# Optimization experiments

Hardware: AMD Instinct MI355X
Metric: run time of the kernel (lower is better)

Reference implementation:

```python
import jax, jax.numpy as jnp
import numpy as np

NUM_HEADS = 8
DIM_HEAD = 48
SCALE = DIM_HEAD ** -0.5


def setup_inputs() -> dict:
    key = jax.random.key(0)
    k1, k2, k3 = jax.random.split(key, 3)
    B, N, D = 4, 2048, 384
    inner = NUM_HEADS * DIM_HEAD  # 384
    x = jax.random.normal(k1, (B, N, D), dtype=jnp.float32)
    # store weights in [in, out] layout (equivalent to torch Linear W.T)
    Wqkv = jax.random.normal(k2, (D, 3 * inner), dtype=jnp.float32) * (D ** -0.5)
    Wproj = jax.random.normal(k3, (inner, D), dtype=jnp.float32) * (inner ** -0.5)
    bproj = jnp.zeros((D,), dtype=jnp.float32)
    return {"x": x, "Wqkv": Wqkv, "Wproj": Wproj, "bproj": bproj}


def reference(x, Wqkv, Wproj, bproj):
    B, N, D = x.shape
    h, dh = NUM_HEADS, DIM_HEAD
    C = h * dh
    # fused QKV projection (qkv_bias=False)
    qkv = (x @ Wqkv).reshape(B, N, 3, h, dh)
    q = qkv[:, :, 0].transpose(0, 2, 1, 3)  # [B, h, N, dh]
    k = qkv[:, :, 1].transpose(0, 2, 1, 3)
    v = qkv[:, :, 2].transpose(0, 2, 1, 3)
    # naive attention: materialize [B, h, N, N] scores
    sim = jnp.einsum("bhqd,bhkd->bhqk", q, k) * SCALE
    attn = jax.nn.softmax(sim, axis=-1)
    out = jnp.einsum("bhqk,bhkd->bhqd", attn, v)  # [B, h, N, dh]
    out = out.transpose(0, 2, 1, 3).reshape(B, N, C)
    return out @ Wproj + bproj
```

## Files before the change

### kernel.cpp

```cpp
#include <hip/hip_runtime.h>
#include <hip/hip_bf16.h>


typedef _Float16 f16x8 __attribute__((ext_vector_type(8)));
typedef _Float16 f16x4 __attribute__((ext_vector_type(4)));
typedef _Float16 f16x2 __attribute__((ext_vector_type(2)));
typedef float    f32x4 __attribute__((ext_vector_type(4)));
typedef float    f32x16 __attribute__((ext_vector_type(16)));

#define QSCL 0.20822035963448658f

static __device__ __forceinline__ f16x2 cvt_pk_f16(float a, float b) {
    return __builtin_bit_cast(f16x2, __builtin_amdgcn_cvt_pkrtz(a, b));
}

__global__ __launch_bounds__(256) void prep(const float4* __restrict__ x,
                                            const float* __restrict__ wq,
                                            const float* __restrict__ wp,
                                            f16x4* __restrict__ xh4,
                                            _Float16* __restrict__ wqt,
                                            _Float16* __restrict__ wpt)
{
    __shared__ _Float16 t[64][65];
    const int blk = blockIdx.x, tid = threadIdx.x;
    if (blk < 144) {
        const float* src; _Float16* dst; int Nn, k0, n0;
        if (blk < 108) {
            src = wq; dst = wqt; Nn = 1152;
            k0 = (blk % 6) * 64; n0 = (blk / 6) * 64;
        } else {
            const int b2 = blk - 108;
            src = wp; dst = wpt; Nn = 384;
            k0 = (b2 % 6) * 64; n0 = (b2 / 6) * 64;
        }
        #pragma unroll
        for (int i = 0; i < 16; i++) {
            const int id = tid + i * 256;
            const int k = id >> 6, n = id & 63;
            t[k][n] = (_Float16)src[(size_t)(k0 + k) * Nn + n0 + n];
        }
        __syncthreads();
        #pragma unroll
        for (int i = 0; i < 16; i++) {
            const int id = tid + i * 256;
            const int n = id >> 6, k = id & 63;
            dst[(size_t)(n0 + n) * 384 + k0 + k] = t[k][n];
        }
    } else {
        const int base = (blk - 144) * 3072;
        #pragma unroll
        for (int r = 0; r < 12; r++) {
            const int j = base + r * 256 + tid;
            const float4 tt = x[j];
            f16x4 hh;
            hh[0] = (_Float16)tt.x; hh[1] = (_Float16)tt.y;
            hh[2] = (_Float16)tt.z; hh[3] = (_Float16)tt.w;
            xh4[j] = hh;
        }
    }
}

union QkvSmem {
    struct { _Float16 As[128][40]; _Float16 Bs[128][40]; } g;
    _Float16 Ts[128][136];
    _Float16 Ts2[128][136];
};

__global__ __launch_bounds__(256) void qkv_f16(const _Float16* __restrict__ A,
                                               const _Float16* __restrict__ Bt,
                                               _Float16* __restrict__ qh,
                                               _Float16* __restrict__ kh,
                                               _Float16* __restrict__ vt)
{
    __shared__ QkvSmem sm;
    const int tid = threadIdx.x;
    const int w = tid >> 6, lane = tid & 63, cl = lane & 15, quad = lane >> 4;
    const int bm = blockIdx.x, bn = blockIdx.y;

    f32x4 acc[2][8];
    const f32x4 z4 = {0.f, 0.f, 0.f, 0.f};
    #pragma unroll
    for (int mi = 0; mi < 2; mi++)
        #pragma unroll
        for (int t = 0; t < 8; t++) acc[mi][t] = z4;

    const int ar = tid >> 2, ac = (tid & 3) * 8;
    const _Float16* Ag = A  + (size_t)(bm * 128 + ar) * 384 + ac;
    const _Float16* Bg = Bt + (size_t)(bn * 128 + ar) * 384 + ac;

    f16x8 pa[2], pb[2];
    #pragma unroll
    for (int j = 0; j < 2; j++) {
        pa[j] = *(const f16x8*)(Ag + (size_t)(64 * j) * 384);
        pb[j] = *(const f16x8*)(Bg + (size_t)(64 * j) * 384);
    }

    for (int k0 = 0; k0 < 384; k0 += 32) {
        __syncthreads();
        #pragma unroll
        for (int j = 0; j < 2; j++) {
            *(f16x8*)&sm.g.As[ar + 64 * j][ac] = pa[j];
            *(f16x8*)&sm.g.Bs[ar + 64 * j][ac] = pb[j];
        }
        __syncthreads();
        if (k0 + 32 < 384) {
            #pragma unroll
            for (int j = 0; j < 2; j++) {
                pa[j] = *(const f16x8*)(Ag + (size_t)(64 * j) * 384 + k0 + 32);
                pb[j] = *(const f16x8*)(Bg + (size_t)(64 * j) * 384 + k0 + 32);
            }
        }
        f16x8 bf[8];
        #pragma unroll
        for (int t = 0; t < 8; t++)
            bf[t] = *(const f16x8*)&sm.g.Bs[t * 16 + cl][quad * 8];
        #pragma unroll
        for (int mi = 0; mi < 2; mi++) {
            const f16x8 af = *(const f16x8*)&sm.g.As[w * 32 + mi * 16 + cl][quad * 8];
            #pragma unroll
            for (int t = 0; t < 8; t++)
                acc[mi][t] = __builtin_amdgcn_mfma_f32_16x16x32_f16(af, bf[t], acc[mi][t], 0, 0, 0);
        }
    }

    const int s = (bn * 128) / 384;
    const int b  = (bm * 128) >> 11;
    const int n0 = (bm * 128) & 2047;
    if (s == 2) {
        __syncthreads();
        const int qp = ((quad & 1) << 1) | (quad >> 1);
        #pragma unroll
        for (int t = 0; t < 8; t++)
            #pragma unroll
            for (int mi = 0; mi < 2; mi++)
                #pragma unroll
                for (int r = 0; r < 4; r++)
                    sm.Ts[t * 16 + cl][w * 32 + mi * 16 + qp * 4 + r] =
                        (_Float16)acc[mi][t][r];
        __syncthreads();
        const int colbase = bn * 128 - 768;
        #pragma unroll
        for (int i = 0; i < 8; i++) {
            const int c = i * 256 + tid;
            const int col = c >> 4, nc = c & 15;
            const int gcol = colbase + col;
            const int head = gcol / 48, d = gcol - head * 48;
            const int bh = b * 8 + head;
            *(f16x8*)&vt[(size_t)(bh * 48 + d) * 2048 + n0 + nc * 8] =
                *(const f16x8*)&sm.Ts[col][nc * 8];
        }
    } else {
        __syncthreads();
        const float scl = (s == 0) ? QSCL : 1.0f;
        #pragma unroll
        for (int t = 0; t < 8; t++)
            #pragma unroll
            for (int mi = 0; mi < 2; mi++)
                #pragma unroll
                for (int r = 0; r < 4; r++)
                    sm.Ts2[w * 32 + mi * 16 + quad * 4 + r][t * 16 + cl] =
                        (_Float16)(acc[mi][t][r] * scl);
        __syncthreads();
        _Float16* dst = (s == 0) ? qh : kh;
        const int colbase = bn * 128 - s * 384;
        #pragma unroll
        for (int i = 0; i < 8; i++) {
            const int c = i * 256 + tid;
            const int row = c >> 4, ch = c & 15;
            const int gcol = colbase + ch * 8;
            const int head = gcol / 48, d = gcol - head * 48;
            const int bh = b * 8 + head;
            *(f16x8*)&dst[(size_t)(bh * 2048 + n0 + row) * 48 + d] =
                *(const f16x8*)&sm.Ts2[row][ch * 8];
        }
    }
}

#define KS_S 56
#define VS_S 72

union AttnSmem {
    struct {
        _Float16 Ks[2][64][KS_S];
        _Float16 Vts[2][64][VS_S];
    } a;
    _Float16 Ot[128][58];
};

__global__ __launch_bounds__(256) void attn_f16(const _Float16* __restrict__ qh,
                                                const _Float16* __restrict__ kh,
                                                const _Float16* __restrict__ vt,
                                                _Float16* __restrict__ ab)
{
    __shared__ AttnSmem sm;
    const int tid = threadIdx.x;
    const int w = tid >> 6, lane = tid & 63, ln = lane & 31, h = lane >> 5;
    const int bh = blockIdx.x, qt = blockIdx.y;

    for (int i = tid; i < 2 * 16 * VS_S; i += 256) {
        const int bi = i / (16 * VS_S), j = i - bi * (16 * VS_S);
        const int r = 48 + j / VS_S, c = j - (j / VS_S) * VS_S;
        sm.a.Vts[bi][r][c] = (r == 48) ? (_Float16)1.0f : (_Float16)0.0f;
    }

    f16x8 qf[3];
    {
        const _Float16* qp = qh + (size_t)(bh * 2048 + qt * 128 + w * 32 + ln) * 48 + 8 * h;
        qf[0] = *(const f16x8*)qp;
        qf[1] = *(const f16x8*)(qp + 16);
        qf[2] = *(const f16x8*)(qp + 32);
    }

    f32x16 o0, o1;
    #pragma unroll
    for (int r = 0; r < 16; r++) { o0[r] = 0.f; o1[r] = 0.f; }

    const _Float16* kbase = kh + (size_t)bh * 2048 * 48;
    const _Float16* vbase = vt + (size_t)bh * 48 * 2048;

    const int kr0 = tid / 6,        kc0 = (tid % 6) * 8;
    const int kid1 = tid + 256;
    const int kr1 = kid1 / 6,       kc1 = (kid1 % 6) * 8;
    const int vr0 = tid >> 3,       vc0 = (tid & 7) * 8;
    const int vr1 = vr0 + 32;
    const _Float16* ks0 = kbase + (size_t)kr0 * 48 + kc0;
    const _Float16* ks1 = kbase + (size_t)kr1 * 48 + kc1;
    const _Float16* vs0 = vbase + (size_t)vr0 * 2048 + vc0;
    const _Float16* vs1 = vbase + (size_t)vr1 * 2048 + vc0;

    f16x8 rk0 = *(const f16x8*)ks0;
    f16x8 rv0 = *(const f16x8*)vs0;
    f16x8 rk1, rv1;
    if (tid < 128) { rk1 = *(const f16x8*)ks1; rv1 = *(const f16x8*)vs1; }

    for (int t = 0; t < 32; ++t) {
        _Float16 (*Ksb)[KS_S] = sm.a.Ks[t & 1];
        _Float16 (*Vtb)[VS_S] = sm.a.Vts[t & 1];

        *(f16x8*)&Ksb[kr0][kc0] = rk0;
        *(f16x8*)&Vtb[vr0][vc0] = rv0;
        if (tid < 128) {
            *(f16x8*)&Ksb[kr1][kc1] = rk1;
            *(f16x8*)&Vtb[vr1][vc0] = rv1;
        }
        __syncthreads();

        if (t < 31) {
            const int off = (t + 1) * 64;
            rk0 = *(const f16x8*)(ks0 + (size_t)off * 48);
            rv0 = *(const f16x8*)(vs0 + off);
            if (tid < 128) {
                rk1 = *(const f16x8*)(ks1 + (size_t)off * 48);
                rv1 = *(const f16x8*)(vs1 + off);
            }
        }

        f32x16 s0, s1;
        #pragma unroll
        for (int r = 0; r < 16; r++) { s0[r] = 0.f; s1[r] = 0.f; }
        __builtin_amdgcn_s_setprio(1);
        #pragma unroll
        for (int i = 0; i < 3; i++) {
            const f16x8 ka0 = *(const f16x8*)&Ksb[ln][16 * i + 8 * h];
            s0 = __builtin_amdgcn_mfma_f32_32x32x16_f16(ka0, qf[i], s0, 0, 0, 0);
            const f16x8 ka1 = *(const f16x8*)&Ksb[32 + ln][16 * i + 8 * h];
            s1 = __builtin_amdgcn_mfma_f32_32x32x16_f16(ka1, qf[i], s1, 0, 0, 0);
        }
        __builtin_amdgcn_s_setprio(0);

        f16x8 pbf[4];
        f16x2* pp = (f16x2*)pbf;
        #pragma unroll
        for (int m = 0; m < 4; m++) {
            pp[m]      = cvt_pk_f16(
                __builtin_amdgcn_exp2f(s0[2 * m]),     __builtin_amdgcn_exp2f(s0[2 * m + 1]));
            pp[4 + m]  = cvt_pk_f16(
                __builtin_amdgcn_exp2f(s0[8 + 2 * m]), __builtin_amdgcn_exp2f(s0[9 + 2 * m]));
            pp[8 + m]  = cvt_pk_f16(
                __builtin_amdgcn_exp2f(s1[2 * m]),     __builtin_amdgcn_exp2f(s1[2 * m + 1]));
            pp[12 + m] = cvt_pk_f16(
                __builtin_amdgcn_exp2f(s1[8 + 2 * m]), __builtin_amdgcn_exp2f(s1[9 + 2 * m]));
        }

        __builtin_amdgcn_s_setprio(1);
        #pragma unroll
        for (int c = 0; c < 4; c++) {
            const f16x8 av0 = *(const f16x8*)&Vtb[ln][16 * c + 8 * h];
            o0 = __builtin_amdgcn_mfma_f32_32x32x16_f16(av0, pbf[c], o0, 0, 0, 0);
            const f16x8 av1 = *(const f16x8*)&Vtb[32 + ln][16 * c + 8 * h];
            o1 = __builtin_amdgcn_mfma_f32_32x32x16_f16(av1, pbf[c], o1, 0, 0, 0);
        }
        __builtin_amdgcn_s_setprio(0);
    }

    const float lr  = __shfl(o1[8], ln);
    const float inv = 1.f / lr;

    __syncthreads();
    #pragma unroll
    for (int r = 0; r < 16; r++)
        sm.Ot[w * 32 + ln][(r & 3) + 8 * (r >> 2) + 4 * h] = (_Float16)(o0[r] * inv);
    #pragma unroll
    for (int r = 0; r < 8; r++)
        sm.Ot[w * 32 + ln][32 + (r & 3) + 8 * (r >> 2) + 4 * h] = (_Float16)(o1[r] * inv);
    __syncthreads();
    const int b = bh >> 3, hd = bh & 7;
    #pragma unroll
    for (int i = 0; i < 3; i++) {
        const int c2 = i * 256 + tid;
        const int row = c2 / 6, ch = c2 % 6;
        const int q = qt * 128 + row;
        *(f16x8*)&ab[(size_t)(b * 2048 + q) * 384 + hd * 48 + ch * 8] =
            *(const f16x8*)&sm.Ot[row][ch * 8];
    }
}

__global__ __launch_bounds__(256) void proj_f16(const _Float16* __restrict__ A,
                                                const _Float16* __restrict__ Bt,
                                                const float* __restrict__ bias,
                                                float* __restrict__ out)
{
    __shared__ _Float16 As[64][72];
    __shared__ _Float16 Bs[64][72];
    const int tid = threadIdx.x;
    const int w = tid >> 6, lane = tid & 63, cl = lane & 15, quad = lane >> 4;
    const int bm = blockIdx.x, bn = blockIdx.y;

    f32x4 acc[4];
    const f32x4 z4 = {0.f, 0.f, 0.f, 0.f};
    #pragma unroll
    for (int t = 0; t < 4; t++) acc[t] = z4;

    const int ar = tid >> 3, ac = (tid & 7) * 8;
    const _Float16* Ag = A  + (size_t)(bm * 64 + ar) * 384 + ac;
    const _Float16* Bg = Bt + (size_t)(bn * 64 + ar) * 384 + ac;

    f16x8 pa[2], pb[2];
    #pragma unroll
    for (int j = 0; j < 2; j++) {
        pa[j] = *(const f16x8*)(Ag + (size_t)(32 * j) * 384);
        pb[j] = *(const f16x8*)(Bg + (size_t)(32 * j) * 384);
    }

    for (int k0 = 0; k0 < 384; k0 += 64) {
        __syncthreads();
        #pragma unroll
        for (int j = 0; j < 2; j++) {
            *(f16x8*)&As[ar + 32 * j][ac] = pa[j];
            *(f16x8*)&Bs[ar + 32 * j][ac] = pb[j];
        }
        __syncthreads();
        if (k0 + 64 < 384) {
            #pragma unroll
            for (int j = 0; j < 2; j++) {
                pa[j] = *(const f16x8*)(Ag + (size_t)(32 * j) * 384 + k0 + 64);
                pb[j] = *(const f16x8*)(Bg + (size_t)(32 * j) * 384 + k0 + 64);
            }
        }
        #pragma unroll
        for (int kh2 = 0; kh2 < 2; kh2++) {
            const f16x8 af = *(const f16x8*)&As[w * 16 + cl][kh2 * 32 + quad * 8];
            #pragma unroll
            for (int t = 0; t < 4; t++) {
                const f16x8 bf = *(const f16x8*)&Bs[t * 16 + cl][kh2 * 32 + quad * 8];
                acc[t] = __builtin_amdgcn_mfma_f32_16x16x32_f16(af, bf, acc[t], 0, 0, 0);
            }
        }
    }

    #pragma unroll
    for (int t = 0; t < 4; t++) {
        const int col = bn * 64 + t * 16 + cl;
        const float bv = bias[col];
        #pragma unroll
        for (int r = 0; r < 4; r++) {
            const int row = bm * 64 + w * 16 + quad * 4 + r;
            out[(size_t)row * 384 + col] = acc[t][r] + bv;
        }
    }
}

extern "C" void kernel_launch(void* const* d_in, const int* in_sizes, int n_in,
                              void* d_out, int out_size, void* d_ws, size_t ws_size,
                              hipStream_t stream) {
    const float* x     = (const float*)d_in[0];
    const float* Wqkv  = (const float*)d_in[1];
    const float* Wproj = (const float*)d_in[2];
    const float* bproj = (const float*)d_in[3];
    float* out = (float*)d_out;

    char* ws = (char*)d_ws;
    _Float16* xh     = (_Float16*)(ws + 0);
    _Float16* wqkvt  = (_Float16*)(ws + 6291456);
    _Float16* wprojt = (_Float16*)(ws + 7176192);
    _Float16* qh     = (_Float16*)(ws + 7471104);
    _Float16* kh     = (_Float16*)(ws + 13762560);
    _Float16* vt     = (_Float16*)(ws + 20054016);
    _Float16* ab     = (_Float16*)(ws + 26345472);

    prep<<<400, 256, 0, stream>>>((const float4*)x, Wqkv, Wproj,
                                  (f16x4*)xh, wqkvt, wprojt);
    qkv_f16<<<dim3(64, 9), 256, 0, stream>>>(xh, wqkvt, qh, kh, vt);
    attn_f16<<<dim3(32, 16), 256, 0, stream>>>(qh, kh, vt, ab);
    proj_f16<<<dim3(128, 6), 256, 0, stream>>>(ab, wprojt, bproj, out);
}
```

Measured before the change: 133.3 us.

## Split attention key range across two wave groups and merge partial outputs

```diff
diff --git a/kernel.cpp b/kernel.cpp
--- a/kernel.cpp
+++ b/kernel.cpp
@@ -181,13 +181,17 @@
 
 union AttnSmem {
     struct {
-        _Float16 Ks[2][64][KS_S];
-        _Float16 Vts[2][64][VS_S];
+        _Float16 Ks[2][2][64][KS_S];
+        _Float16 Vts[2][2][64][VS_S];
     } a;
-    _Float16 Ot[128][58];
+    struct {
+        float    Of[128][52];
+        float    lv[128];
+        _Float16 Ot[128][58];
+    } e;
 };
 
-__global__ __launch_bounds__(256) void attn_f16(const _Float16* __restrict__ qh,
+__global__ __launch_bounds__(512) void attn_f16(const _Float16* __restrict__ qh,
                                                 const _Float16* __restrict__ kh,
                                                 const _Float16* __restrict__ vt,
                                                 _Float16* __restrict__ ab)
@@ -195,17 +199,22 @@
     __shared__ AttnSmem sm;
     const int tid = threadIdx.x;
     const int w = tid >> 6, lane = tid & 63, ln = lane & 31, h = lane >> 5;
+    const int g = w >> 2, wg = w & 3;
+    const int tid2 = tid & 255;
     const int bh = blockIdx.x, qt = blockIdx.y;
 
-    for (int i = tid; i < 2 * 16 * VS_S; i += 256) {
-        const int bi = i / (16 * VS_S), j = i - bi * (16 * VS_S);
-        const int r = 48 + j / VS_S, c = j - (j / VS_S) * VS_S;
-        sm.a.Vts[bi][r][c] = (r == 48) ? (_Float16)1.0f : (_Float16)0.0f;
+    for (int i = tid; i < 2 * 2 * 16 * VS_S; i += 512) {
+        const int gi = i / (2 * 16 * VS_S);
+        const int j  = i - gi * (2 * 16 * VS_S);
+        const int bi = j / (16 * VS_S);
+        const int j2 = j - bi * (16 * VS_S);
+        const int r = 48 + j2 / VS_S, c = j2 % VS_S;
+        sm.a.Vts[gi][bi][r][c] = (r == 48) ? (_Float16)1.0f : (_Float16)0.0f;
     }
 
     f16x8 qf[3];
     {
-        const _Float16* qp = qh + (size_t)(bh * 2048 + qt * 128 + w * 32 + ln) * 48 + 8 * h;
+        const _Float16* qp = qh + (size_t)(bh * 2048 + qt * 128 + wg * 32 + ln) * 48 + 8 * h;
         qf[0] = *(const f16x8*)qp;
         qf[1] = *(const f16x8*)(qp + 16);
         qf[2] = *(const f16x8*)(qp + 32);
@@ -215,13 +224,13 @@
     #pragma unroll
     for (int r = 0; r < 16; r++) { o0[r] = 0.f; o1[r] = 0.f; }
 
-    const _Float16* kbase = kh + (size_t)bh * 2048 * 48;
-    const _Float16* vbase = vt + (size_t)bh * 48 * 2048;
-
-    const int kr0 = tid / 6,        kc0 = (tid % 6) * 8;
-    const int kid1 = tid + 256;
-    const int kr1 = kid1 / 6,       kc1 = (kid1 % 6) * 8;
-    const int vr0 = tid >> 3,       vc0 = (tid & 7) * 8;
+    const _Float16* kbase = kh + (size_t)bh * 2048 * 48 + (size_t)g * 1024 * 48;
+    const _Float16* vbase = vt + (size_t)bh * 48 * 2048 + g * 1024;
+
+    const int kr0 = tid2 / 6,        kc0 = (tid2 % 6) * 8;
+    const int kid1 = tid2 + 256;
+    const int kr1 = kid1 / 6,        kc1 = (kid1 % 6) * 8;
+    const int vr0 = tid2 >> 3,       vc0 = (tid2 & 7) * 8;
     const int vr1 = vr0 + 32;
     const _Float16* ks0 = kbase + (size_t)kr0 * 48 + kc0;
     const _Float16* ks1 = kbase + (size_t)kr1 * 48 + kc1;
@@ -231,25 +240,25 @@
     f16x8 rk0 = *(const f16x8*)ks0;
     f16x8 rv0 = *(const f16x8*)vs0;
     f16x8 rk1, rv1;
-    if (tid < 128) { rk1 = *(const f16x8*)ks1; rv1 = *(const f16x8*)vs1; }
-
-    for (int t = 0; t < 32; ++t) {
-        _Float16 (*Ksb)[KS_S] = sm.a.Ks[t & 1];
-        _Float16 (*Vtb)[VS_S] = sm.a.Vts[t & 1];
+    if (tid2 < 128) { rk1 = *(const f16x8*)ks1; rv1 = *(const f16x8*)vs1; }
+
+    for (int t = 0; t < 16; ++t) {
+        _Float16 (*Ksb)[KS_S] = sm.a.Ks[g][t & 1];
+        _Float16 (*Vtb)[VS_S] = sm.a.Vts[g][t & 1];
 
         *(f16x8*)&Ksb[kr0][kc0] = rk0;
         *(f16x8*)&Vtb[vr0][vc0] = rv0;
-        if (tid < 128) {
+        if (tid2 < 128) {
             *(f16x8*)&Ksb[kr1][kc1] = rk1;
             *(f16x8*)&Vtb[vr1][vc0] = rv1;
         }
         __syncthreads();
 
-        if (t < 31) {
+        if (t < 15) {
             const int off = (t + 1) * 64;
             rk0 = *(const f16x8*)(ks0 + (size_t)off * 48);
             rv0 = *(const f16x8*)(vs0 + off);
-            if (tid < 128) {
+            if (tid2 < 128) {
                 rk1 = *(const f16x8*)(ks1 + (size_t)off * 48);
                 rv1 = *(const f16x8*)(vs1 + off);
             }
@@ -293,25 +302,57 @@
         __builtin_amdgcn_s_setprio(0);
     }
 
-    const float lr  = __shfl(o1[8], ln);
-    const float inv = 1.f / lr;
+    const float lown = __shfl(o1[8], ln);
 
     __syncthreads();
-    #pragma unroll
-    for (int r = 0; r < 16; r++)
-        sm.Ot[w * 32 + ln][(r & 3) + 8 * (r >> 2) + 4 * h] = (_Float16)(o0[r] * inv);
-    #pragma unroll
-    for (int r = 0; r < 8; r++)
-        sm.Ot[w * 32 + ln][32 + (r & 3) + 8 * (r >> 2) + 4 * h] = (_Float16)(o1[r] * inv);
+
+    const int row = wg * 32 + ln;
+    if (g == 1) {
+        #pragma unroll
+        for (int q4 = 0; q4 < 4; q4++) {
+            f32x4 tq = { o0[4 * q4], o0[4 * q4 + 1], o0[4 * q4 + 2], o0[4 * q4 + 3] };
+            *(f32x4*)&sm.e.Of[row][8 * q4 + 4 * h] = tq;
+        }
+        #pragma unroll
+        for (int q4 = 0; q4 < 2; q4++) {
+            f32x4 tq = { o1[4 * q4], o1[4 * q4 + 1], o1[4 * q4 + 2], o1[4 * q4 + 3] };
+            *(f32x4*)&sm.e.Of[row][32 + 8 * q4 + 4 * h] = tq;
+        }
+        if (h == 0) sm.e.lv[row] = o1[8];
+    }
     __syncthreads();
-    const int b = bh >> 3, hd = bh & 7;
-    #pragma unroll
-    for (int i = 0; i < 3; i++) {
-        const int c2 = i * 256 + tid;
-        const int row = c2 / 6, ch = c2 % 6;
-        const int q = qt * 128 + row;
-        *(f16x8*)&ab[(size_t)(b * 2048 + q) * 384 + hd * 48 + ch * 8] =
-            *(const f16x8*)&sm.Ot[row][ch * 8];
+    if (g == 0) {
+        #pragma unroll
+        for (int q4 = 0; q4 < 4; q4++) {
+            const f32x4 tq = *(const f32x4*)&sm.e.Of[row][8 * q4 + 4 * h];
+            o0[4 * q4] += tq[0]; o0[4 * q4 + 1] += tq[1];
+            o0[4 * q4 + 2] += tq[2]; o0[4 * q4 + 3] += tq[3];
+        }
+        #pragma unroll
+        for (int q4 = 0; q4 < 2; q4++) {
+            const f32x4 tq = *(const f32x4*)&sm.e.Of[row][32 + 8 * q4 + 4 * h];
+            o1[4 * q4] += tq[0]; o1[4 * q4 + 1] += tq[1];
+            o1[4 * q4 + 2] += tq[2]; o1[4 * q4 + 3] += tq[3];
+        }
+        const float inv = 1.f / (lown + sm.e.lv[row]);
+        #pragma unroll
+        for (int r = 0; r < 16; r++)
+            sm.e.Ot[row][(r & 3) + 8 * (r >> 2) + 4 * h] = (_Float16)(o0[r] * inv);
+        #pragma unroll
+        for (int r = 0; r < 8; r++)
+            sm.e.Ot[row][32 + (r & 3) + 8 * (r >> 2) + 4 * h] = (_Float16)(o1[r] * inv);
+    }
+    __syncthreads();
+    if (g == 0) {
+        const int b = bh >> 3, hd = bh & 7;
+        #pragma unroll
+        for (int i = 0; i < 3; i++) {
+            const int c2 = i * 256 + tid;
+            const int rw = c2 / 6, ch = c2 % 6;
+            const int q = qt * 128 + rw;
+            *(f16x8*)&ab[(size_t)(b * 2048 + q) * 384 + hd * 48 + ch * 8] =
+                *(const f16x8*)&sm.e.Ot[rw][ch * 8];
+        }
     }
 }
 
@@ -401,6 +442,6 @@
     prep<<<400, 256, 0, stream>>>((const float4*)x, Wqkv, Wproj,
                                   (f16x4*)xh, wqkvt, wprojt);
     qkv_f16<<<dim3(64, 9), 256, 0, stream>>>(xh, wqkvt, qh, kh, vt);
-    attn_f16<<<dim3(32, 16), 256, 0, stream>>>(qh, kh, vt, ab);
+    attn_f16<<<dim3(32, 16), 512, 0, stream>>>(qh, kh, vt, ab);
     proj_f16<<<dim3(128, 6), 256, 0, stream>>>(ab, wprojt, bproj, out);
 }
```

After: 130.2 us. -2.3%, faster.
